# Kernel optimization log

Measured on AMD Instinct MI355X. Metric: run time of the kernel, lower is better.

Reference implementation:

```python
import jax, jax.numpy as jnp
import numpy as np

DIM = 2048
THRESH = 0.33

def _ternary(w):
    # sign() with dead zone: {-1, 0, +1}; detached from grad (matches torch.no_grad)
    return jax.lax.stop_gradient(jnp.where(jnp.abs(w) < THRESH, 0.0, jnp.sign(w)))

def _bitlinear(x, w, b):
    # F.linear(x, ternary_w, bias): x @ ternary_w.T + b
    return jnp.einsum('bsd,od->bso', x, _ternary(w)) + b

def setup_inputs() -> dict:
    key = jax.random.key(0)
    ks = jax.random.split(key, 6)
    B, S, D = 8, 2048, DIM
    x = jax.random.normal(ks[0], (B, S, D), dtype=jnp.float32)
    h_prev = jax.random.normal(ks[1], (B, S, D), dtype=jnp.float32)
    # BitLinear reset_parameters: uniform(-1, 1); bias zeros
    wf = jax.random.uniform(ks[2], (D, D), minval=-1.0, maxval=1.0, dtype=jnp.float32)
    wc = jax.random.uniform(ks[3], (D, D), minval=-1.0, maxval=1.0, dtype=jnp.float32)
    wg = jax.random.uniform(ks[4], (D, D), minval=-1.0, maxval=1.0, dtype=jnp.float32)
    wo = jax.random.uniform(ks[5], (D, D), minval=-1.0, maxval=1.0, dtype=jnp.float32)
    bf = jnp.zeros((D,), dtype=jnp.float32)
    bc = jnp.zeros((D,), dtype=jnp.float32)
    bg = jnp.zeros((D,), dtype=jnp.float32)
    bo = jnp.zeros((D,), dtype=jnp.float32)
    return {"x": x, "h_prev": h_prev, "wf": wf, "bf": bf, "wc": wc, "bc": bc,
            "wg": wg, "bg": bg, "wo": wo, "bo": bo}

def reference(x, h_prev, wf, bf, wc, bc, wg, bg, wo, bo):
    f = jax.nn.sigmoid(_bitlinear(x, wf, bf))
    c = jax.nn.silu(_bitlinear(x, wc, bc))
    h = f * h_prev + (1.0 - f) * c
    g = jax.nn.sigmoid(_bitlinear(x, wg, bg))
    o = _bitlinear(g * h, wo, bo)
    return (o, h)
```

## Files before the change

### kernel.cpp

```cpp
#include <hip/hip_runtime.h>
#include <hip/hip_bf16.h>
#include <cstdint>

#define DIM   2048
#define MROWS 16384

typedef __bf16 bf16x8 __attribute__((ext_vector_type(8)));
typedef float  f32x4  __attribute__((ext_vector_type(4)));
typedef unsigned short u16;
typedef unsigned int   u32;


__device__ __forceinline__ u16 ternary_bits(float w) {
    u32 u = __float_as_uint(w);
    u16 s = (u16)((u >> 16) & 0x8000u);
    return (__builtin_fabsf(w) < 0.33f) ? (u16)0 : (u16)(0x3F80u | s);
}

__device__ __forceinline__ u16 f2bf_rne(float f) {
    u32 u = __float_as_uint(f);
    u32 r = (u + 0x7FFFu + ((u >> 16) & 1u)) >> 16;
    return (u16)r;
}

__device__ __forceinline__ void gload16(const void* g, void* l) {
    __builtin_amdgcn_global_load_lds(
        (const __attribute__((address_space(1))) void*)g,
        (__attribute__((address_space(3))) void*)l,
        16, 0, 0);
}


__global__ void prep_weights(const float* __restrict__ wf, const float* __restrict__ wc,
                             const float* __restrict__ wg, const float* __restrict__ wo,
                             u16* __restrict__ out) {
    const float* srcs[4] = {wf, wc, wg, wo};
    const float* src = srcs[blockIdx.y];
    u16* dst = out + (size_t)blockIdx.y * (DIM * DIM);
    int e = (blockIdx.x * 256 + threadIdx.x) * 8;
    float4 v0 = *(const float4*)(src + e);
    float4 v1 = *(const float4*)(src + e + 4);
    ushort4 o0, o1;
    o0.x = ternary_bits(v0.x); o0.y = ternary_bits(v0.y);
    o0.z = ternary_bits(v0.z); o0.w = ternary_bits(v0.w);
    o1.x = ternary_bits(v1.x); o1.y = ternary_bits(v1.y);
    o1.z = ternary_bits(v1.z); o1.w = ternary_bits(v1.w);
    *(ushort4*)(dst + e)     = o0;
    *(ushort4*)(dst + e + 4) = o1;
}

__global__ void cast_x(const float* __restrict__ x, u16* __restrict__ xb) {
    size_t e = ((size_t)blockIdx.x * 256 + threadIdx.x) * 8;
    float4 v0 = *(const float4*)(x + e);
    float4 v1 = *(const float4*)(x + e + 4);
    ushort4 o0, o1;
    o0.x = f2bf_rne(v0.x); o0.y = f2bf_rne(v0.y);
    o0.z = f2bf_rne(v0.z); o0.w = f2bf_rne(v0.w);
    o1.x = f2bf_rne(v1.x); o1.y = f2bf_rne(v1.y);
    o1.z = f2bf_rne(v1.z); o1.w = f2bf_rne(v1.w);
    *(ushort4*)(xb + e)     = o0;
    *(ushort4*)(xb + e + 4) = o1;
}


__global__ __launch_bounds__(512) void gemm1(
    const u16* __restrict__ xb,
    const u16* __restrict__ wt,
    const float* __restrict__ bfv_, const float* __restrict__ bcv_, const float* __restrict__ bgv_,
    const float* __restrict__ hprev,
    float* __restrict__ hout,
    u16* __restrict__ gh)
{
    __shared__ __align__(16) u16 sA[2][128 * 64];
    __shared__ __align__(16) u16 sB[2][3 * 128 * 64];

    const int tid  = threadIdx.x;
    const int lane = tid & 63;
    const int wave = tid >> 6;
    const int wr   = wave >> 2;
    const int wc   = wave & 3;

    const int bid  = blockIdx.x;
    const int swz  = (bid & 7) * 256 + (bid >> 3);
    const int brow = (swz & 127) * 128;
    const int bcol = (swz >> 7) * 128;

    const int srow = tid >> 3;
    const int cg   = (tid & 7) ^ (srow & 7);
    const int sc_l = (tid & 7) * 8;

    f32x4 acc[3][4][2] = {};

    auto stage = [&](int buf, int kt) {
        #pragma unroll
        for (int i = 0; i < 2; ++i) {
            const u16* src = xb + (size_t)(brow + i * 64 + srow) * DIM + kt + cg * 8;
            gload16(src, &sA[buf][(i * 64 + srow) * 64 + sc_l]);
        }
        #pragma unroll
        for (int j = 0; j < 6; ++j) {
            const int m  = j >> 1;
            const int rl = (j & 1) * 64 + srow;
            const u16* src = wt + (size_t)m * DIM * DIM + (size_t)(bcol + rl) * DIM + kt + cg * 8;
            gload16(src, &sB[buf][m * 8192 + rl * 64 + sc_l]);
        }
    };

    stage(0, 0);
    __syncthreads();

    int cur = 0;
    for (int kt = 0; kt < DIM; kt += 64) {
        if (kt + 64 < DIM) stage(cur ^ 1, kt + 64);

        const u16* lA = &sA[cur][0];
        const u16* lB = &sB[cur][0];
        #pragma unroll
        for (int ks = 0; ks < 2; ++ks) {
            const int hi = lane >> 4;
            const int cs = ((ks * 4 + hi) ^ (lane & 7)) * 8;
            bf16x8 a[4];
            #pragma unroll
            for (int mi = 0; mi < 4; ++mi) {
                const int ra = wr * 64 + mi * 16 + (lane & 15);
                a[mi] = *(const bf16x8*)(lA + ra * 64 + cs);
            }
            __builtin_amdgcn_s_setprio(1);
            #pragma unroll
            for (int m = 0; m < 3; ++m) {
                #pragma unroll
                for (int ni = 0; ni < 2; ++ni) {
                    const int rb = wc * 32 + ni * 16 + (lane & 15);
                    bf16x8 b = *(const bf16x8*)(lB + m * 8192 + rb * 64 + cs);
                    #pragma unroll
                    for (int mi = 0; mi < 4; ++mi)
                        acc[m][mi][ni] = __builtin_amdgcn_mfma_f32_16x16x32_bf16(a[mi], b, acc[m][mi][ni], 0, 0, 0);
                }
            }
            __builtin_amdgcn_s_setprio(0);
        }
        __syncthreads();
        cur ^= 1;
    }

    const int colbase = bcol + wc * 32 + (lane & 15);
    const int rowbase = brow + wr * 64 + ((lane >> 4) * 4);
    #pragma unroll
    for (int ni = 0; ni < 2; ++ni) {
        const int col = colbase + ni * 16;
        const float bfv = bfv_[col], bcv = bcv_[col], bgv = bgv_[col];
        #pragma unroll
        for (int mi = 0; mi < 4; ++mi) {
            #pragma unroll
            for (int j = 0; j < 4; ++j) {
                const int row = rowbase + mi * 16 + j;
                const size_t idx = (size_t)row * DIM + col;
                float pf = acc[0][mi][ni][j] + bfv;
                float pc = acc[1][mi][ni][j] + bcv;
                float pg = acc[2][mi][ni][j] + bgv;
                float f = 1.f / (1.f + __expf(-pf));
                float c = pc / (1.f + __expf(-pc));
                float g = 1.f / (1.f + __expf(-pg));
                float h = f * hprev[idx] + (1.f - f) * c;
                hout[idx] = h;
                gh[idx] = f2bf_rne(g * h);
            }
        }
    }
}


__global__ __launch_bounds__(256) void gemm2(
    const u16* __restrict__ gh,
    const u16* __restrict__ wot,
    const float* __restrict__ bov_,
    float* __restrict__ oout)
{
    __shared__ __align__(16) u16 sA[2][128 * 64];
    __shared__ __align__(16) u16 sB[2][128 * 64];

    const int tid  = threadIdx.x;
    const int lane = tid & 63;
    const int wave = tid >> 6;
    const int wr   = wave >> 1;
    const int wc   = wave & 1;

    const int bid  = blockIdx.x;
    const int swz  = (bid & 7) * 256 + (bid >> 3);
    const int brow = (swz & 127) * 128;
    const int bcol = (swz >> 7) * 128;

    const int srow = tid >> 3;
    const int cg   = (tid & 7) ^ (srow & 7);
    const int sc_l = (tid & 7) * 8;

    f32x4 acc[4][4] = {};

    auto stage = [&](int buf, int kt) {
        #pragma unroll
        for (int i = 0; i < 4; ++i) {
            const int rl = i * 32 + srow;
            const u16* srcA = gh  + (size_t)(brow + rl) * DIM + kt + cg * 8;
            const u16* srcB = wot + (size_t)(bcol + rl) * DIM + kt + cg * 8;
            gload16(srcA, &sA[buf][rl * 64 + sc_l]);
            gload16(srcB, &sB[buf][rl * 64 + sc_l]);
        }
    };

    stage(0, 0);
    __syncthreads();

    int cur = 0;
    for (int kt = 0; kt < DIM; kt += 64) {
        if (kt + 64 < DIM) stage(cur ^ 1, kt + 64);

        const u16* lA = &sA[cur][0];
        const u16* lB = &sB[cur][0];
        #pragma unroll
        for (int ks = 0; ks < 2; ++ks) {
            const int hi = lane >> 4;
            const int cs = ((ks * 4 + hi) ^ (lane & 7)) * 8;
            bf16x8 a[4], b[4];
            #pragma unroll
            for (int mi = 0; mi < 4; ++mi)
                a[mi] = *(const bf16x8*)(lA + (wr * 64 + mi * 16 + (lane & 15)) * 64 + cs);
            #pragma unroll
            for (int ni = 0; ni < 4; ++ni)
                b[ni] = *(const bf16x8*)(lB + (wc * 64 + ni * 16 + (lane & 15)) * 64 + cs);
            __builtin_amdgcn_s_setprio(1);
            #pragma unroll
            for (int mi = 0; mi < 4; ++mi)
                #pragma unroll
                for (int ni = 0; ni < 4; ++ni)
                    acc[mi][ni] = __builtin_amdgcn_mfma_f32_16x16x32_bf16(a[mi], b[ni], acc[mi][ni], 0, 0, 0);
            __builtin_amdgcn_s_setprio(0);
        }
        __syncthreads();
        cur ^= 1;
    }

    const int colbase = bcol + wc * 64 + (lane & 15);
    const int rowbase = brow + wr * 64 + ((lane >> 4) * 4);
    #pragma unroll
    for (int ni = 0; ni < 4; ++ni) {
        const int col = colbase + ni * 16;
        const float bov = bov_[col];
        #pragma unroll
        for (int mi = 0; mi < 4; ++mi) {
            #pragma unroll
            for (int j = 0; j < 4; ++j) {
                const int row = rowbase + mi * 16 + j;
                oout[(size_t)row * DIM + col] = acc[mi][ni][j] + bov;
            }
        }
    }
}

extern "C" void kernel_launch(void* const* d_in, const int* in_sizes, int n_in,
                              void* d_out, int out_size, void* d_ws, size_t ws_size,
                              hipStream_t stream) {
    const float* x  = (const float*)d_in[0];
    const float* hp = (const float*)d_in[1];
    const float* wf = (const float*)d_in[2];
    const float* bf = (const float*)d_in[3];
    const float* wc = (const float*)d_in[4];
    const float* bc = (const float*)d_in[5];
    const float* wg = (const float*)d_in[6];
    const float* bg = (const float*)d_in[7];
    const float* wo = (const float*)d_in[8];
    const float* bo = (const float*)d_in[9];

    float* o_out = (float*)d_out;
    float* h_out = o_out + (size_t)MROWS * DIM;

    u16* w_t  = (u16*)d_ws;
    u16* x_bf = (u16*)((char*)d_ws + 33554432);
    u16* gh   = (u16*)((char*)d_ws + 100663296);

    prep_weights<<<dim3(2048, 4), 256, 0, stream>>>(wf, wc, wg, wo, w_t);
    cast_x<<<dim3(16384), 256, 0, stream>>>(x, x_bf);
    gemm1<<<dim3(2048), 512, 0, stream>>>(x_bf, w_t, bf, bc, bg, hp, h_out, gh);
    gemm2<<<dim3(2048), 256, 0, stream>>>(gh, w_t + 3 * (size_t)DIM * DIM, bo, o_out);
}
```

Baseline: 831.5 us.

## Interleave LDS reads, global loads and MFMA with fine-grained barrier schedule

Both GEMMs now use a hand-scheduled main loop. Each 64-wide K tile is split into two 32-wide halves with a new LDS swizzle, and global-to-LDS loads for the next tile are issued in slices between MFMA phases, with explicit vmcnt waits and raw s_barrier in place of __syncthreads. gemm2 moves to 512 threads with 128x256 tiles and half as many blocks, so each A tile is reused across more output columns. The aim is to hide memory latency and cut synchronisation stalls, at the cost of many extra barriers and fragile hand-tuned wait counts.

```diff
diff --git a/kernel.cpp b/kernel.cpp
--- a/kernel.cpp
+++ b/kernel.cpp
@@ -4,11 +4,15 @@
 
 #define DIM   2048
 #define MROWS 16384
+#define NT    32
 
 typedef __bf16 bf16x8 __attribute__((ext_vector_type(8)));
 typedef float  f32x4  __attribute__((ext_vector_type(4)));
 typedef unsigned short u16;
 typedef unsigned int   u32;
+
+#define BARRIER() asm volatile("s_barrier" ::: "memory")
+#define WAITVM(N) asm volatile("s_waitcnt vmcnt(" #N ")" ::: "memory")
 
 
 __device__ __forceinline__ u16 ternary_bits(float w) {
@@ -71,189 +75,272 @@
     float* __restrict__ hout,
     u16* __restrict__ gh)
 {
-    __shared__ __align__(16) u16 sA[2][128 * 64];
-    __shared__ __align__(16) u16 sB[2][3 * 128 * 64];
+    __shared__ __align__(16) u16 sA[2][2][128 * 32];
+    __shared__ __align__(16) u16 sB[2][2][3][128 * 32];
 
     const int tid  = threadIdx.x;
     const int lane = tid & 63;
     const int wave = tid >> 6;
     const int wr   = wave >> 2;
-    const int wc   = wave & 3;
+    const int wcq  = wave & 3;
 
     const int bid  = blockIdx.x;
     const int swz  = (bid & 7) * 256 + (bid >> 3);
     const int brow = (swz & 127) * 128;
     const int bcol = (swz >> 7) * 128;
 
-    const int srow = tid >> 3;
-    const int cg   = (tid & 7) ^ (srow & 7);
-    const int sc_l = (tid & 7) * 8;
-
-    f32x4 acc[3][4][2] = {};
-
-    auto stage = [&](int buf, int kt) {
-        #pragma unroll
-        for (int i = 0; i < 2; ++i) {
-            const u16* src = xb + (size_t)(brow + i * 64 + srow) * DIM + kt + cg * 8;
-            gload16(src, &sA[buf][(i * 64 + srow) * 64 + sc_l]);
-        }
-        #pragma unroll
-        for (int j = 0; j < 6; ++j) {
-            const int m  = j >> 1;
-            const int rl = (j & 1) * 64 + srow;
-            const u16* src = wt + (size_t)m * DIM * DIM + (size_t)(bcol + rl) * DIM + kt + cg * 8;
-            gload16(src, &sB[buf][m * 8192 + rl * 64 + sc_l]);
-        }
-    };
-
-    stage(0, 0);
-    __syncthreads();
-
-    int cur = 0;
-    for (int kt = 0; kt < DIM; kt += 64) {
-        if (kt + 64 < DIM) stage(cur ^ 1, kt + 64);
-
-        const u16* lA = &sA[cur][0];
-        const u16* lB = &sB[cur][0];
-        #pragma unroll
-        for (int ks = 0; ks < 2; ++ks) {
-            const int hi = lane >> 4;
-            const int cs = ((ks * 4 + hi) ^ (lane & 7)) * 8;
-            bf16x8 a[4];
+    const int row512 = tid >> 2;
+    const int gc4    = (tid & 3) ^ ((tid >> 3) & 3);
+    const int ldst   = tid * 8;
+
+    const int fr  = lane & 15;
+    const int hi  = lane >> 4;
+    const int csw = (hi ^ ((fr >> 1) & 3)) * 8;
+
+    f32x4 acc0[3][4] = {};
+    f32x4 acc1[3][4] = {};
+
+    const u16* aSrc  = xb + (size_t)(brow + row512) * DIM;
+    const u16* bSrc0 = wt + (size_t)(bcol + row512) * DIM;
+    const size_t WSTRIDE = (size_t)DIM * DIM;
+
+    auto issueA = [&](int buf, int kt, int ks) {
+        gload16(aSrc + kt + ks * 32 + gc4 * 8, (u16*)&sA[buf][ks][ldst]);
+    };
+    auto issueB = [&](int buf, int kt, int g, int ks) {
+        gload16(bSrc0 + (size_t)g * WSTRIDE + kt + ks * 32 + gc4 * 8,
+                (u16*)&sB[buf][ks][g][ldst]);
+    };
+
+    auto rdA = [&](const u16* lA, int ks, bf16x8 (&a)[4]) {
+        #pragma unroll
+        for (int mi = 0; mi < 4; ++mi)
+            a[mi] = *(const bf16x8*)(lA + ks * 4096 + (wr * 64 + mi * 16 + fr) * 32 + csw);
+    };
+    auto rdB = [&](const u16* lB, int ks, int ni, bf16x8 (&b)[3]) {
+        #pragma unroll
+        for (int g = 0; g < 3; ++g)
+            b[g] = *(const bf16x8*)(lB + ks * 12288 + g * 4096 + (wcq * 32 + ni * 16 + fr) * 32 + csw);
+    };
+    auto domfma = [&](bf16x8 (&a)[4], bf16x8 (&b)[3], f32x4 (&c)[3][4]) {
+        __builtin_amdgcn_s_setprio(1);
+        #pragma unroll
+        for (int g = 0; g < 3; ++g)
             #pragma unroll
-            for (int mi = 0; mi < 4; ++mi) {
-                const int ra = wr * 64 + mi * 16 + (lane & 15);
-                a[mi] = *(const bf16x8*)(lA + ra * 64 + cs);
-            }
-            __builtin_amdgcn_s_setprio(1);
-            #pragma unroll
-            for (int m = 0; m < 3; ++m) {
-                #pragma unroll
-                for (int ni = 0; ni < 2; ++ni) {
-                    const int rb = wc * 32 + ni * 16 + (lane & 15);
-                    bf16x8 b = *(const bf16x8*)(lB + m * 8192 + rb * 64 + cs);
-                    #pragma unroll
-                    for (int mi = 0; mi < 4; ++mi)
-                        acc[m][mi][ni] = __builtin_amdgcn_mfma_f32_16x16x32_bf16(a[mi], b, acc[m][mi][ni], 0, 0, 0);
-                }
-            }
-            __builtin_amdgcn_s_setprio(0);
-        }
-        __syncthreads();
-        cur ^= 1;
+            for (int mi = 0; mi < 4; ++mi)
+                c[g][mi] = __builtin_amdgcn_mfma_f32_16x16x32_bf16(a[mi], b[g], c[g][mi], 0, 0, 0);
+        __builtin_amdgcn_s_setprio(0);
+    };
+
+    issueA(0, 0, 0); issueB(0, 0, 0, 0);
+    issueB(0, 0, 1, 0); issueB(0, 0, 2, 0);
+    issueA(0, 0, 1); issueB(0, 0, 0, 1);
+    issueB(0, 0, 1, 1); issueB(0, 0, 2, 1);
+    WAITVM(0);
+    BARRIER();
+
+    #pragma unroll 1
+    for (int t = 0; t < NT - 1; ++t) {
+        const u16* lA = &sA[t & 1][0][0];
+        const u16* lB = &sB[t & 1][0][0][0];
+        const int nb = (t + 1) & 1;
+        const int kn = (t + 1) * 64;
+        bf16x8 a[4], b[3];
+        rdA(lA, 0, a); rdB(lB, 0, 0, b);
+        issueA(nb, kn, 0); issueB(nb, kn, 0, 0);
+        BARRIER();
+        domfma(a, b, acc0);
+        BARRIER();
+        rdB(lB, 0, 1, b);
+        issueB(nb, kn, 1, 0); issueB(nb, kn, 2, 0);
+        WAITVM(4);
+        BARRIER();
+        domfma(a, b, acc1);
+        BARRIER();
+        rdA(lA, 1, a); rdB(lB, 1, 0, b);
+        issueA(nb, kn, 1); issueB(nb, kn, 0, 1);
+        BARRIER();
+        domfma(a, b, acc0);
+        BARRIER();
+        rdB(lB, 1, 1, b);
+        issueB(nb, kn, 1, 1); issueB(nb, kn, 2, 1);
+        WAITVM(4);
+        BARRIER();
+        domfma(a, b, acc1);
+        BARRIER();
     }
-
-    const int colbase = bcol + wc * 32 + (lane & 15);
-    const int rowbase = brow + wr * 64 + ((lane >> 4) * 4);
-    #pragma unroll
-    for (int ni = 0; ni < 2; ++ni) {
-        const int col = colbase + ni * 16;
+    {
+        const u16* lA = &sA[1][0][0];
+        const u16* lB = &sB[1][0][0][0];
+        bf16x8 a[4], b[3];
+        rdA(lA, 0, a); rdB(lB, 0, 0, b);
+        BARRIER(); domfma(a, b, acc0); BARRIER();
+        rdB(lB, 0, 1, b);
+        WAITVM(0);
+        BARRIER(); domfma(a, b, acc1); BARRIER();
+        rdA(lA, 1, a); rdB(lB, 1, 0, b);
+        BARRIER(); domfma(a, b, acc0); BARRIER();
+        rdB(lB, 1, 1, b);
+        domfma(a, b, acc1);
+    }
+
+    auto epi = [&](int ni, f32x4 (&c)[3][4]) {
+        const int col = bcol + wcq * 32 + ni * 16 + fr;
         const float bfv = bfv_[col], bcv = bcv_[col], bgv = bgv_[col];
         #pragma unroll
         for (int mi = 0; mi < 4; ++mi) {
             #pragma unroll
             for (int j = 0; j < 4; ++j) {
-                const int row = rowbase + mi * 16 + j;
+                const int row = brow + wr * 64 + mi * 16 + hi * 4 + j;
                 const size_t idx = (size_t)row * DIM + col;
-                float pf = acc[0][mi][ni][j] + bfv;
-                float pc = acc[1][mi][ni][j] + bcv;
-                float pg = acc[2][mi][ni][j] + bgv;
-                float f = 1.f / (1.f + __expf(-pf));
-                float c = pc / (1.f + __expf(-pc));
-                float g = 1.f / (1.f + __expf(-pg));
-                float h = f * hprev[idx] + (1.f - f) * c;
+                float pf = c[0][mi][j] + bfv;
+                float pc = c[1][mi][j] + bcv;
+                float pg = c[2][mi][j] + bgv;
+                float f  = 1.f / (1.f + __expf(-pf));
+                float cc = pc / (1.f + __expf(-pc));
+                float g  = 1.f / (1.f + __expf(-pg));
+                float h  = f * hprev[idx] + (1.f - f) * cc;
                 hout[idx] = h;
                 gh[idx] = f2bf_rne(g * h);
             }
         }
-    }
-}
-
-
-__global__ __launch_bounds__(256) void gemm2(
+    };
+    epi(0, acc0);
+    epi(1, acc1);
+}
+
+
+__global__ __launch_bounds__(512) void gemm2(
     const u16* __restrict__ gh,
     const u16* __restrict__ wot,
     const float* __restrict__ bov_,
     float* __restrict__ oout)
 {
-    __shared__ __align__(16) u16 sA[2][128 * 64];
-    __shared__ __align__(16) u16 sB[2][128 * 64];
+    __shared__ __align__(16) u16 sA[2][2][128 * 32];
+    __shared__ __align__(16) u16 sB[2][2][256 * 32];
 
     const int tid  = threadIdx.x;
     const int lane = tid & 63;
     const int wave = tid >> 6;
-    const int wr   = wave >> 1;
-    const int wc   = wave & 1;
+    const int wr   = wave >> 2;
+    const int wcq  = wave & 3;
 
     const int bid  = blockIdx.x;
-    const int swz  = (bid & 7) * 256 + (bid >> 3);
+    const int swz  = (bid & 7) * 128 + (bid >> 3);
     const int brow = (swz & 127) * 128;
-    const int bcol = (swz >> 7) * 128;
-
-    const int srow = tid >> 3;
-    const int cg   = (tid & 7) ^ (srow & 7);
-    const int sc_l = (tid & 7) * 8;
-
-    f32x4 acc[4][4] = {};
-
-    auto stage = [&](int buf, int kt) {
-        #pragma unroll
-        for (int i = 0; i < 4; ++i) {
-            const int rl = i * 32 + srow;
-            const u16* srcA = gh  + (size_t)(brow + rl) * DIM + kt + cg * 8;
-            const u16* srcB = wot + (size_t)(bcol + rl) * DIM + kt + cg * 8;
-            gload16(srcA, &sA[buf][rl * 64 + sc_l]);
-            gload16(srcB, &sB[buf][rl * 64 + sc_l]);
-        }
-    };
-
-    stage(0, 0);
-    __syncthreads();
-
-    int cur = 0;
-    for (int kt = 0; kt < DIM; kt += 64) {
-        if (kt + 64 < DIM) stage(cur ^ 1, kt + 64);
-
-        const u16* lA = &sA[cur][0];
-        const u16* lB = &sB[cur][0];
-        #pragma unroll
-        for (int ks = 0; ks < 2; ++ks) {
-            const int hi = lane >> 4;
-            const int cs = ((ks * 4 + hi) ^ (lane & 7)) * 8;
-            bf16x8 a[4], b[4];
+    const int bcol = (swz >> 7) * 256;
+
+    const int row512 = tid >> 2;
+    const int gc4    = (tid & 3) ^ ((tid >> 3) & 3);
+    const int ldst   = tid * 8;
+
+    const int fr  = lane & 15;
+    const int hi  = lane >> 4;
+    const int csw = (hi ^ ((fr >> 1) & 3)) * 8;
+
+    f32x4 accL[4][2] = {};
+    f32x4 accH[4][2] = {};
+
+    const u16* aSrc  = gh  + (size_t)(brow + row512) * DIM;
+    const u16* bSrcL = wot + (size_t)(bcol + row512) * DIM;
+    const u16* bSrcH = wot + (size_t)(bcol + 128 + row512) * DIM;
+
+    auto issueA = [&](int buf, int kt, int ks) {
+        gload16(aSrc + kt + ks * 32 + gc4 * 8, (u16*)&sA[buf][ks][ldst]);
+    };
+    auto issueBlo = [&](int buf, int kt, int ks) {
+        gload16(bSrcL + kt + ks * 32 + gc4 * 8, (u16*)&sB[buf][ks][ldst]);
+    };
+    auto issueBhi = [&](int buf, int kt, int ks) {
+        gload16(bSrcH + kt + ks * 32 + gc4 * 8, (u16*)&sB[buf][ks][4096 + ldst]);
+    };
+
+    auto rdA = [&](const u16* lA, int ks, bf16x8 (&a)[4]) {
+        #pragma unroll
+        for (int mi = 0; mi < 4; ++mi)
+            a[mi] = *(const bf16x8*)(lA + ks * 4096 + (wr * 64 + mi * 16 + fr) * 32 + csw);
+    };
+    auto rdB2 = [&](const u16* lB, int ks, int nbase, bf16x8 (&b)[2]) {
+        #pragma unroll
+        for (int jn = 0; jn < 2; ++jn)
+            b[jn] = *(const bf16x8*)(lB + ks * 8192 + (wcq * 64 + (nbase + jn) * 16 + fr) * 32 + csw);
+    };
+    auto domfma2 = [&](bf16x8 (&a)[4], bf16x8 (&b)[2], f32x4 (&c)[4][2]) {
+        __builtin_amdgcn_s_setprio(1);
+        #pragma unroll
+        for (int jn = 0; jn < 2; ++jn)
             #pragma unroll
             for (int mi = 0; mi < 4; ++mi)
-                a[mi] = *(const bf16x8*)(lA + (wr * 64 + mi * 16 + (lane & 15)) * 64 + cs);
-            #pragma unroll
-            for (int ni = 0; ni < 4; ++ni)
-                b[ni] = *(const bf16x8*)(lB + (wc * 64 + ni * 16 + (lane & 15)) * 64 + cs);
-            __builtin_amdgcn_s_setprio(1);
+                c[mi][jn] = __builtin_amdgcn_mfma_f32_16x16x32_bf16(a[mi], b[jn], c[mi][jn], 0, 0, 0);
+        __builtin_amdgcn_s_setprio(0);
+    };
+
+    issueA(0, 0, 0); issueBlo(0, 0, 0);
+    issueBhi(0, 0, 0); issueA(0, 0, 1);
+    issueBlo(0, 0, 1);
+    issueBhi(0, 0, 1);
+    WAITVM(0);
+    BARRIER();
+
+    #pragma unroll 1
+    for (int t = 0; t < NT - 1; ++t) {
+        const u16* lA = &sA[t & 1][0][0];
+        const u16* lB = &sB[t & 1][0][0];
+        const int nb = (t + 1) & 1;
+        const int kn = (t + 1) * 64;
+        bf16x8 a[4], b[2];
+        rdA(lA, 0, a); rdB2(lB, 0, 0, b);
+        issueA(nb, kn, 0); issueBlo(nb, kn, 0);
+        BARRIER();
+        domfma2(a, b, accL);
+        BARRIER();
+        rdB2(lB, 0, 2, b);
+        issueBhi(nb, kn, 0); issueA(nb, kn, 1);
+        WAITVM(4);
+        BARRIER();
+        domfma2(a, b, accH);
+        BARRIER();
+        rdA(lA, 1, a); rdB2(lB, 1, 0, b);
+        issueBlo(nb, kn, 1);
+        BARRIER();
+        domfma2(a, b, accL);
+        BARRIER();
+        rdB2(lB, 1, 2, b);
+        issueBhi(nb, kn, 1);
+        WAITVM(3);
+        BARRIER();
+        domfma2(a, b, accH);
+        BARRIER();
+    }
+    {
+        const u16* lA = &sA[1][0][0];
+        const u16* lB = &sB[1][0][0];
+        bf16x8 a[4], b[2];
+        rdA(lA, 0, a); rdB2(lB, 0, 0, b);
+        BARRIER(); domfma2(a, b, accL); BARRIER();
+        rdB2(lB, 0, 2, b);
+        WAITVM(0);
+        BARRIER(); domfma2(a, b, accH); BARRIER();
+        rdA(lA, 1, a); rdB2(lB, 1, 0, b);
+        BARRIER(); domfma2(a, b, accL); BARRIER();
+        rdB2(lB, 1, 2, b);
+        domfma2(a, b, accH);
+    }
+
+    auto epi2 = [&](int nbase, f32x4 (&c)[4][2]) {
+        #pragma unroll
+        for (int jn = 0; jn < 2; ++jn) {
+            const int col = bcol + wcq * 64 + (nbase + jn) * 16 + fr;
+            const float bov = bov_[col];
             #pragma unroll
             for (int mi = 0; mi < 4; ++mi)
                 #pragma unroll
-                for (int ni = 0; ni < 4; ++ni)
-                    acc[mi][ni] = __builtin_amdgcn_mfma_f32_16x16x32_bf16(a[mi], b[ni], acc[mi][ni], 0, 0, 0);
-            __builtin_amdgcn_s_setprio(0);
+                for (int j = 0; j < 4; ++j)
+                    oout[(size_t)(brow + wr * 64 + mi * 16 + hi * 4 + j) * DIM + col] = c[mi][jn][j] + bov;
         }
-        __syncthreads();
-        cur ^= 1;
-    }
-
-    const int colbase = bcol + wc * 64 + (lane & 15);
-    const int rowbase = brow + wr * 64 + ((lane >> 4) * 4);
-    #pragma unroll
-    for (int ni = 0; ni < 4; ++ni) {
-        const int col = colbase + ni * 16;
-        const float bov = bov_[col];
-        #pragma unroll
-        for (int mi = 0; mi < 4; ++mi) {
-            #pragma unroll
-            for (int j = 0; j < 4; ++j) {
-                const int row = rowbase + mi * 16 + j;
-                oout[(size_t)row * DIM + col] = acc[mi][ni][j] + bov;
-            }
-        }
-    }
+    };
+    epi2(0, accL);
+    epi2(2, accH);
 }
 
 extern "C" void kernel_launch(void* const* d_in, const int* in_sizes, int n_in,
@@ -280,5 +367,5 @@
     prep_weights<<<dim3(2048, 4), 256, 0, stream>>>(wf, wc, wg, wo, w_t);
     cast_x<<<dim3(16384), 256, 0, stream>>>(x, x_bf);
     gemm1<<<dim3(2048), 512, 0, stream>>>(x_bf, w_t, bf, bc, bg, hp, h_out, gh);
-    gemm2<<<dim3(2048), 256, 0, stream>>>(gh, w_t + 3 * (size_t)DIM * DIM, bo, o_out);
-}
+    gemm2<<<dim3(1024), 512, 0, stream>>>(gh, w_t + 3 * (size_t)DIM * DIM, bo, o_out);
+}
```

Result: faster. 801.7 us (-3.6%).
